# Kernel optimization log

Hardware: AMD Instinct MI355X
Metric: run time of the kernel (lower is better)

The kernel has to match this reference:

```python
import jax, jax.numpy as jnp
import numpy as np

EPS = 1e-5

def _bn(x, g, b):
    # BatchNorm3d in training mode over (batch, spatial) dims; x: [B, C, N]
    mean = jnp.mean(x, axis=(0, 2), keepdims=True)
    var = jnp.var(x, axis=(0, 2), keepdims=True)
    return g[None, :, None] * (x - mean) * jax.lax.rsqrt(var + EPS) + b[None, :, None]


def setup_inputs() -> dict:
    key = jax.random.key(0)
    ks = jax.random.split(key, 6)
    B, C, N, K, H = 2, 128, 32768, 9, 512
    x = jax.random.normal(ks[0], (B, C, N, 1), dtype=jnp.float32)
    edge_index = jax.random.randint(ks[1], (2, B, N, K), 0, N, dtype=jnp.int32)
    s = 0.05
    return {
        "x": x,
        "edge_index": edge_index,
        "w_mr": jax.random.normal(ks[2], (C, 2 * C), dtype=jnp.float32) * s,
        "b_mr": jnp.zeros((C,), jnp.float32),
        "g_mr": jnp.ones((C,), jnp.float32),
        "be_mr": jnp.zeros((C,), jnp.float32),
        "w1": jax.random.normal(ks[3], (H, C), dtype=jnp.float32) * s,
        "b1": jnp.zeros((H,), jnp.float32),
        "g1": jnp.ones((H,), jnp.float32),
        "be1": jnp.zeros((H,), jnp.float32),
        "w2": jax.random.normal(ks[4], (C, H), dtype=jnp.float32) * s,
        "b2": jnp.zeros((C,), jnp.float32),
        "g2": jnp.ones((C,), jnp.float32),
        "be2": jnp.zeros((C,), jnp.float32),
    }


def reference(x, edge_index, w_mr, b_mr, g_mr, be_mr, w1, b1, g1, be1, w2, b2, g2, be2):
    # x: [B, C, N, 1], edge_index: [2, B, N, K]
    B, C, N, _ = x.shape
    x2 = x[..., 0]  # [B, C, N]

    # batched_index_select: gather node features along N for each (B, N, K) index
    gather = jax.vmap(lambda xb, ib: xb[:, ib])  # ([C,N],[N,K]) -> [C,N,K]
    x_i = gather(x2, edge_index[1])  # [B, C, N, K] center features
    x_j = gather(x2, edge_index[0])  # [B, C, N, K] neighbor features
    rel = jnp.max(x_j - x_i, axis=-1)  # max-relative reduction -> [B, C, N]

    # torch.cat([x.unsqueeze(2), rel.unsqueeze(2)], 2).reshape(B, 2C, N): interleaved channels
    feat = jnp.stack([x2, rel], axis=2).reshape(B, 2 * C, N)

    # BasicConv([2C, C]): Conv3d 1x1 -> BN -> ReLU
    y = jnp.einsum('oc,bcn->bon', w_mr, feat) + b_mr[None, :, None]
    y = jax.nn.relu(_bn(y, g_mr, be_mr))

    # FFN: conv1x1 C->H, BN, ReLU, conv1x1 H->C, BN, residual
    h = jnp.einsum('hc,bcn->bhn', w1, y) + b1[None, :, None]
    h = jax.nn.relu(_bn(h, g1, be1))
    out = jnp.einsum('ch,bhn->bcn', w2, h) + b2[None, :, None]
    out = _bn(out, g2, be2) + y
    return out  # [B, C, N]
```

## Files before the change

### kernel.cpp

```cpp
#include <hip/hip_runtime.h>
#include <hip/hip_bf16.h>
#include <cstddef>
#include <cstdint>

#define BB 2
#define CC 128
#define NN 32768
#define KNBR 9
#define HH 512
#define PP (BB * NN)
#define TWO_C 256
#define EPSBN 1e-5f

typedef __attribute__((ext_vector_type(4))) float f32x4;
typedef __attribute__((ext_vector_type(8))) short s16x8;

__device__ __forceinline__ float bf2f(unsigned int u) {
    return __uint_as_float(u << 16);
}
__device__ __forceinline__ unsigned short f2bf(float f) {
    unsigned int u = __float_as_uint(f);
    u += 0x7fffu + ((u >> 16) & 1u);
    return (unsigned short)(u >> 16);
}

__device__ __forceinline__ s16x8 bnrelu(s16x8 v, f32x4 sa0, f32x4 sa1,
                                        f32x4 sb0, f32x4 sb1) {
    union { s16x8 s; __hip_bfloat162 h[4]; } u;
    u.s = v;
#pragma unroll
    for (int q = 0; q < 4; q++) {
        const float2 f = __bfloat1622float2(u.h[q]);
        const float slo = (q < 2) ? sa0[2 * q] : sa1[2 * q - 4];
        const float shi = (q < 2) ? sa0[2 * q + 1] : sa1[2 * q - 3];
        const float tlo = (q < 2) ? sb0[2 * q] : sb1[2 * q - 4];
        const float thi = (q < 2) ? sb0[2 * q + 1] : sb1[2 * q - 3];
        u.h[q] = __float22bfloat162_rn(make_float2(
            fmaxf(fmaf(slo, f.x, tlo), 0.f), fmaxf(fmaf(shi, f.y, thi), 0.f)));
    }
    return u.s;
}


__global__ __launch_bounds__(256) void transpose_wconv_kernel(
    const float* __restrict__ x, unsigned short* __restrict__ xT,
    const float* __restrict__ w_mr, const float* __restrict__ w1,
    const float* __restrict__ w2, unsigned short* __restrict__ o_mr,
    unsigned short* __restrict__ o1, unsigned short* __restrict__ o2) {
    if (blockIdx.x >= NN / 32) {
        if (blockIdx.y != 0) return;
        const int t = (blockIdx.x - NN / 32) * 256 + threadIdx.x;
        const float* src; unsigned short* dst; int K; int slot;
        if (t < 8192) { src = w1; dst = o1; K = 128; slot = t; }
        else if (t < 16384) { src = w2; dst = o2; K = 512; slot = t - 8192; }
        else if (t < 20480) { src = w_mr; dst = o_mr; K = 256; slot = t - 16384; }
        else return;
        const int lane = slot & 63;
        const int kt = (slot >> 6) % (K / 32);
        const int ot = (slot >> 6) / (K / 32);
        const int oc = ot * 16 + (lane & 15);
        const int k0 = kt * 32 + (lane >> 4) * 8;
        s16x8 v;
#pragma unroll
        for (int j = 0; j < 8; j++) v[j] = (short)f2bf(src[(size_t)oc * K + k0 + j]);
        *(s16x8*)(dst + (size_t)slot * 8) = v;
        return;
    }
    __shared__ float t[32][129];
    const int b = blockIdx.y;
    const int n0 = blockIdx.x * 32;
    const int tid = threadIdx.x;
    {
        const int tn = tid % 32;
        const int cq = tid / 32;
        for (int c = cq; c < CC; c += 8)
            t[tn][c] = x[((size_t)b * CC + c) * NN + n0 + tn];
    }
    __syncthreads();
    {
        const int ct = tid % 128;
        const int nq = tid / 128;
        for (int nl = nq; nl < 32; nl += 2)
            xT[((size_t)b * NN + n0 + nl) * CC + ct] = f2bf(t[nl][ct]);
    }
}

__global__ __launch_bounds__(256) void gather_kernel(
    const unsigned short* __restrict__ xT, const int* __restrict__ ei,
    unsigned short* __restrict__ feat) {
    __shared__ unsigned short lds[16 * 264];
    const int p0 = blockIdx.x * 16;
    const int b = p0 >> 15;
    const int n0 = p0 & (NN - 1);
    const int tid = threadIdx.x;
    const int wv = tid >> 6, lane = tid & 63;
    const unsigned short* xb = xT + (size_t)b * NN * CC;

#pragma unroll
    for (int q = 0; q < 4; q++) {
        const int pl = wv * 4 + q;
        const int n = n0 + pl;
        const int* e0 = ei + ((size_t)b * NN + n) * KNBR;
        const int* e1 = ei + ((size_t)(BB + b) * NN + n) * KNBR;
        const unsigned int xv = *(const unsigned int*)(xb + (size_t)n * CC + lane * 2);
        float m0 = -INFINITY, m1 = -INFINITY;
#pragma unroll
        for (int k = 0; k < KNBR; k++) {
            const int j0 = e0[k], j1 = e1[k];
            const unsigned int va = *(const unsigned int*)(xb + (size_t)j0 * CC + lane * 2);
            const unsigned int vb = *(const unsigned int*)(xb + (size_t)j1 * CC + lane * 2);
            m0 = fmaxf(m0, bf2f(va & 0xffffu) - bf2f(vb & 0xffffu));
            m1 = fmaxf(m1, bf2f(va >> 16) - bf2f(vb >> 16));
        }
        ushort4 o;
        o.x = (unsigned short)(xv & 0xffffu);
        o.y = f2bf(m0);
        o.z = (unsigned short)(xv >> 16);
        o.w = f2bf(m1);
        *(ushort4*)(lds + pl * 264 + lane * 4) = o;
    }
    __syncthreads();
#pragma unroll
    for (int pass = 0; pass < 2; pass++) {
        const int s = pass * 256 + tid;
        const int kt = s >> 6, ln = s & 63;
        const int pl = ln & 15, kq = ln >> 4;
        const s16x8 v = *(const s16x8*)(lds + pl * 264 + kt * 32 + kq * 8);
        *(s16x8*)(feat + ((size_t)((p0 >> 4) * 8 + kt) * 64 + ln) * 8) = v;
    }
}

template <int KTOT, int OCB, int OC, bool ACT>
__global__ __launch_bounds__(256, 2) void sgemm2_kernel(
    const unsigned short* __restrict__ A,
    const unsigned short* __restrict__ W,
    const float* __restrict__ bias,
    const float* __restrict__ act,
    unsigned short* __restrict__ Cout,
    float* __restrict__ part) {
    constexpr int KT = KTOT / 32;
    constexpr int NTB = OCB / 16;
    constexpr int NTW = NTB / 2;
    constexpr int OCT32 = OC / 32;

    __shared__ __align__(16) unsigned short ALDS[4 * KT * 512];
    __shared__ float bs[4 * OCB];

    const int tid = threadIdx.x;
    const int w = tid >> 6, lane = tid & 63;
    const int mw = w >> 1, nw = w & 1;
    const int lm = lane & 15, lg = lane >> 4;
    const int pt0 = blockIdx.x * 4;
    const int ob = blockIdx.y * OCB;

    {
        const unsigned short* Asrc = A + (size_t)pt0 * KT * 512;
        s16x8 ar[KT];
#pragma unroll
        for (int i = 0; i < KT; i++)
            ar[i] = *(const s16x8*)(Asrc + (size_t)(i * 256 + tid) * 8);
        if (ACT) {
#pragma unroll
            for (int i = 0; i < KT; i++) {
                const int s = i * 256 + tid;
                const int kts = (s >> 6) % KT;
                const int lgs = (s & 63) >> 4;
                const int ke = kts * 32 + lgs * 8;
                const f32x4 xa0 = *(const f32x4*)(act + ke);
                const f32x4 xa1 = *(const f32x4*)(act + ke + 4);
                const f32x4 xb0 = *(const f32x4*)(act + KTOT + ke);
                const f32x4 xb1 = *(const f32x4*)(act + KTOT + ke + 4);
                ar[i] = bnrelu(ar[i], xa0, xa1, xb0, xb1);
            }
        }
#pragma unroll
        for (int i = 0; i < KT; i++)
            *(s16x8*)(ALDS + (size_t)(i * 256 + tid) * 8) = ar[i];
    }
    __syncthreads();

    f32x4 acc[2][NTW] = {};

#pragma unroll
    for (int kt = 0; kt < KT; kt++) {
        s16x8 bF[NTW];
#pragma unroll
        for (int n = 0; n < NTW; n++)
            bF[n] = *(const s16x8*)(
                W + ((size_t)(((ob >> 4) + nw * NTW + n) * KT + kt) * 64 + lane) * 8);
        const s16x8 a0 = *(const s16x8*)(ALDS + (size_t)(((mw * 2 + 0) * KT + kt) * 64 + lane) * 8);
        const s16x8 a1 = *(const s16x8*)(ALDS + (size_t)(((mw * 2 + 1) * KT + kt) * 64 + lane) * 8);
#pragma unroll
        for (int n = 0; n < NTW; n++) {
            acc[0][n] = __builtin_amdgcn_mfma_f32_16x16x32_bf16(a0, bF[n], acc[0][n], 0, 0, 0);
            acc[1][n] = __builtin_amdgcn_mfma_f32_16x16x32_bf16(a1, bF[n], acc[1][n], 0, 0, 0);
        }
    }
    __syncthreads();

    unsigned short* myct = ALDS + (size_t)w * (NTW / 2) * 512;
    float sA[NTW], sB[NTW], bo[NTW];
#pragma unroll
    for (int n = 0; n < NTW; n++) {
        sA[n] = 0.f; sB[n] = 0.f;
        bo[n] = bias[ob + nw * (OCB / 2) + n * 16 + lm];
    }
#pragma unroll
    for (int mi = 0; mi < 2; mi++) {
        const int ptile = pt0 + mw * 2 + mi;
#pragma unroll
        for (int n = 0; n < NTW; n++) {
            const int lbase = ((n & 1) * 2 + (lm >> 3)) * 16 + lg * 4;
            const int elem = lm & 7;
#pragma unroll
            for (int j = 0; j < 4; j++) {
                const float h = acc[mi][n][j] + bo[n];
                sA[n] += h;
                sB[n] = fmaf(h, h, sB[n]);
                myct[(size_t)((n >> 1) * 64 + lbase + j) * 8 + elem] = f2bf(h);
            }
        }
#pragma unroll
        for (int og = 0; og < NTW / 2; og++) {
            const s16x8 v = *(const s16x8*)(myct + (size_t)(og * 64 + lane) * 8);
            const int oct = ((ob + nw * (OCB / 2)) >> 5) + og;
            *(s16x8*)(Cout + ((size_t)(ptile * OCT32 + oct) * 64 + lane) * 8) = v;
        }
    }
#pragma unroll
    for (int n = 0; n < NTW; n++) {
        float a = sA[n], q = sB[n];
        a += __shfl_xor(a, 16); a += __shfl_xor(a, 32);
        q += __shfl_xor(q, 16); q += __shfl_xor(q, 32);
        if (lg == 0) {
            const int chl = nw * (OCB / 2) + n * 16 + lm;
            bs[(mw * 2 + 0) * OCB + chl] = a;
            bs[(mw * 2 + 1) * OCB + chl] = q;
        }
    }
    __syncthreads();
    if (tid < OCB) {
        const float s = bs[0 * OCB + tid] + bs[2 * OCB + tid];
        const float q = bs[1 * OCB + tid] + bs[3 * OCB + tid];
        const size_t o = ((size_t)blockIdx.y * gridDim.x + blockIdx.x) * 2 * OCB;
        part[o + tid] = s;
        part[o + OCB + tid] = q;
    }
}

template <int OCB, int GX>
__global__ __launch_bounds__(256) void reduce_kernel(
    const float* __restrict__ part, const float* __restrict__ g,
    const float* __restrict__ be, float* __restrict__ act, int OC, float invP) {
    __shared__ float ls[4], lq[4];
    const int c = blockIdx.x;
    const int by = c / OCB, co = c % OCB;
    const int tid = threadIdx.x;
    float s = 0.f, q = 0.f;
#pragma unroll
    for (int i = 0; i < GX / 256; i++) {
        const int bx = i * 256 + tid;
        const size_t o = (size_t)(by * GX + bx) * 2 * OCB;
        s += part[o + co];
        q += part[o + OCB + co];
    }
#pragma unroll
    for (int off = 32; off >= 1; off >>= 1) {
        s += __shfl_xor(s, off);
        q += __shfl_xor(q, off);
    }
    if ((tid & 63) == 0) { ls[tid >> 6] = s; lq[tid >> 6] = q; }
    __syncthreads();
    if (tid == 0) {
        s = ls[0] + ls[1] + ls[2] + ls[3];
        q = lq[0] + lq[1] + lq[2] + lq[3];
        const float mean = s * invP;
        const float var = q * invP - mean * mean;
        const float a = g[c] * rsqrtf(var + EPSBN);
        act[c] = a;
        act[OC + c] = be[c] - mean * a;
    }
}

__global__ __launch_bounds__(256) void final_kernel(
    const unsigned short* __restrict__ yF, const unsigned short* __restrict__ oF,
    const float* __restrict__ act1, const float* __restrict__ act3,
    float* __restrict__ out) {
    __shared__ float t[32][132];
    const int p0 = blockIdx.x * 32;
    const int b = p0 >> 15;
    const int n0 = p0 & (NN - 1);
    const int tid = threadIdx.x;
#pragma unroll
    for (int s = tid; s < 512; s += 256) {
        const int pt = s >> 8;
        const int kt = (s >> 6) & 3;
        const int lane = s & 63;
        const int nl = pt * 16 + (lane & 15);
        const int c0 = kt * 32 + (lane >> 4) * 8;
        const size_t off = ((size_t)(((p0 >> 4) + pt) * 4 + kt) * 64 + lane) * 8;
        const s16x8 yv = *(const s16x8*)(yF + off);
        const s16x8 ov = *(const s16x8*)(oF + off);
        const f32x4 a1lo = *(const f32x4*)(act1 + c0);
        const f32x4 a1hi = *(const f32x4*)(act1 + c0 + 4);
        const f32x4 b1lo = *(const f32x4*)(act1 + CC + c0);
        const f32x4 b1hi = *(const f32x4*)(act1 + CC + c0 + 4);
        const f32x4 a3lo = *(const f32x4*)(act3 + c0);
        const f32x4 a3hi = *(const f32x4*)(act3 + c0 + 4);
        const f32x4 b3lo = *(const f32x4*)(act3 + CC + c0);
        const f32x4 b3hi = *(const f32x4*)(act3 + CC + c0 + 4);
#pragma unroll
        for (int j = 0; j < 8; j++) {
            const float yf = bf2f((unsigned short)yv[j]);
            const float of = bf2f((unsigned short)ov[j]);
            const float a1 = (j < 4) ? a1lo[j] : a1hi[j - 4];
            const float b1 = (j < 4) ? b1lo[j] : b1hi[j - 4];
            const float a3 = (j < 4) ? a3lo[j] : a3hi[j - 4];
            const float b3 = (j < 4) ? b3lo[j] : b3hi[j - 4];
            t[nl][c0 + j] = fmaf(a3, of, b3) + fmaxf(fmaf(a1, yf, b1), 0.f);
        }
    }
    __syncthreads();
    const int tn = tid & 31;
    const int cq = tid >> 5;
    for (int c = cq; c < CC; c += 8)
        out[((size_t)b * CC + c) * NN + n0 + tn] = t[tn][c];
}

extern "C" void kernel_launch(void* const* d_in, const int* in_sizes, int n_in,
                              void* d_out, int out_size, void* d_ws, size_t ws_size,
                              hipStream_t stream) {
    const float* x     = (const float*)d_in[0];
    const int*   ei    = (const int*)d_in[1];
    const float* w_mr  = (const float*)d_in[2];
    const float* b_mr  = (const float*)d_in[3];
    const float* g_mr  = (const float*)d_in[4];
    const float* be_mr = (const float*)d_in[5];
    const float* w1    = (const float*)d_in[6];
    const float* b1    = (const float*)d_in[7];
    const float* g1    = (const float*)d_in[8];
    const float* be1   = (const float*)d_in[9];
    const float* w2    = (const float*)d_in[10];
    const float* b2    = (const float*)d_in[11];
    const float* g2    = (const float*)d_in[12];
    const float* be2   = (const float*)d_in[13];
    float* out = (float*)d_out;

    char* ws = (char*)d_ws;
    unsigned short* xT    = (unsigned short*)(ws + 0);
    unsigned short* featF = (unsigned short*)(ws + 16777216);
    unsigned short* yF    = (unsigned short*)(ws + 50331648);
    unsigned short* hF    = (unsigned short*)(ws + 67108864);
    unsigned short* oF    = (unsigned short*)(ws + 134217728);
    unsigned short* wmrF  = (unsigned short*)(ws + 150994944);
    unsigned short* w1F   = (unsigned short*)(ws + 151060480);
    unsigned short* w2F   = (unsigned short*)(ws + 151191552);
    float* act1  = (float*)(ws + 151322624);
    float* act2  = (float*)(ws + 151323648);
    float* act3  = (float*)(ws + 151327744);
    float* part1 = (float*)(ws + 67108864);
    float* part2 = (float*)(ws + 134217728);
    float* part3 = (float*)(ws + 16777216);

    const float invP = 1.0f / (float)PP;

    transpose_wconv_kernel<<<dim3(NN / 32 + 80, BB), 256, 0, stream>>>(
        x, xT, w_mr, w1, w2, wmrF, w1F, w2F);
    gather_kernel<<<PP / 16, 256, 0, stream>>>(xT, ei, featF);

    sgemm2_kernel<TWO_C, CC, CC, false><<<dim3(PP / 64, 1), 256, 0, stream>>>(
        featF, wmrF, b_mr, act1, yF, part1);
    reduce_kernel<CC, PP / 64><<<CC, 256, 0, stream>>>(
        part1, g_mr, be_mr, act1, CC, invP);

    sgemm2_kernel<CC, 256, HH, true><<<dim3(PP / 64, 2), 256, 0, stream>>>(
        yF, w1F, b1, act1, hF, part2);
    reduce_kernel<256, PP / 64><<<HH, 256, 0, stream>>>(
        part2, g1, be1, act2, HH, invP);

    sgemm2_kernel<HH, CC, CC, true><<<dim3(PP / 64, 1), 256, 0, stream>>>(
        hF, w2F, b2, act2, oF, part3);
    reduce_kernel<CC, PP / 64><<<CC, 256, 0, stream>>>(
        part3, g2, be2, act3, CC, invP);

    final_kernel<<<PP / 32, 256, 0, stream>>>(yF, oF, act1, act3, out);
}
```

Baseline: 152.7 us.

## Fuse neighbor gather/max-relative into first GEMM kernel via LDS staging

Replaces the separate gather kernel and first sgemm with one kernel that computes the max-relative features for 64 points into shared memory, then runs the MFMA GEMM against the mr weights and emits BN partial sums. This removes the write and re-read of the 2C-wide feature buffer in global memory and one launch. In exchange each block serializes gather latency before its MFMA work, with fewer blocks (PP/64 instead of PP/16) to hide the irregular gather loads.

```diff
diff --git a/kernel.cpp b/kernel.cpp
--- a/kernel.cpp
+++ b/kernel.cpp
@@ -85,48 +85,131 @@
     }
 }
 
-__global__ __launch_bounds__(256) void gather_kernel(
+__global__ __launch_bounds__(256, 2) void ggemm1_kernel(
     const unsigned short* __restrict__ xT, const int* __restrict__ ei,
-    unsigned short* __restrict__ feat) {
-    __shared__ unsigned short lds[16 * 264];
-    const int p0 = blockIdx.x * 16;
+    const unsigned short* __restrict__ W,
+    const float* __restrict__ bias,
+    unsigned short* __restrict__ Cout,
+    float* __restrict__ part) {
+    constexpr int KT = TWO_C / 32;
+    constexpr int NTW = 4;
+    constexpr int OCT32 = CC / 32;
+
+    __shared__ __align__(16) unsigned short ALDS[4 * KT * 512];
+    __shared__ __align__(16) unsigned short scr[16 * 264];
+    __shared__ float bs[4 * CC];
+
+    const int tid = threadIdx.x;
+    const int w = tid >> 6, lane = tid & 63;
+    const int mw = w >> 1, nw = w & 1;
+    const int lm = lane & 15, lg = lane >> 4;
+    const int p0 = blockIdx.x * 64;
     const int b = p0 >> 15;
     const int n0 = p0 & (NN - 1);
-    const int tid = threadIdx.x;
-    const int wv = tid >> 6, lane = tid & 63;
+    const int pt0 = blockIdx.x * 4;
     const unsigned short* xb = xT + (size_t)b * NN * CC;
 
-#pragma unroll
-    for (int q = 0; q < 4; q++) {
-        const int pl = wv * 4 + q;
-        const int n = n0 + pl;
-        const int* e0 = ei + ((size_t)b * NN + n) * KNBR;
-        const int* e1 = ei + ((size_t)(BB + b) * NN + n) * KNBR;
-        const unsigned int xv = *(const unsigned int*)(xb + (size_t)n * CC + lane * 2);
-        float m0 = -INFINITY, m1 = -INFINITY;
-#pragma unroll
-        for (int k = 0; k < KNBR; k++) {
-            const int j0 = e0[k], j1 = e1[k];
-            const unsigned int va = *(const unsigned int*)(xb + (size_t)j0 * CC + lane * 2);
-            const unsigned int vb = *(const unsigned int*)(xb + (size_t)j1 * CC + lane * 2);
-            m0 = fmaxf(m0, bf2f(va & 0xffffu) - bf2f(vb & 0xffffu));
-            m1 = fmaxf(m1, bf2f(va >> 16) - bf2f(vb >> 16));
-        }
-        ushort4 o;
-        o.x = (unsigned short)(xv & 0xffffu);
-        o.y = f2bf(m0);
-        o.z = (unsigned short)(xv >> 16);
-        o.w = f2bf(m1);
-        *(ushort4*)(lds + pl * 264 + lane * 4) = o;
-    }
-    __syncthreads();
-#pragma unroll
-    for (int pass = 0; pass < 2; pass++) {
-        const int s = pass * 256 + tid;
-        const int kt = s >> 6, ln = s & 63;
-        const int pl = ln & 15, kq = ln >> 4;
-        const s16x8 v = *(const s16x8*)(lds + pl * 264 + kt * 32 + kq * 8);
-        *(s16x8*)(feat + ((size_t)((p0 >> 4) * 8 + kt) * 64 + ln) * 8) = v;
+    for (int it = 0; it < 4; it++) {
+#pragma unroll
+        for (int q = 0; q < 4; q++) {
+            const int spl = w * 4 + q;
+            const int n = n0 + it * 16 + spl;
+            const int* e0 = ei + ((size_t)b * NN + n) * KNBR;
+            const int* e1 = ei + ((size_t)(BB + b) * NN + n) * KNBR;
+            const unsigned int xv = *(const unsigned int*)(xb + (size_t)n * CC + lane * 2);
+            float m0 = -INFINITY, m1 = -INFINITY;
+#pragma unroll
+            for (int k = 0; k < KNBR; k++) {
+                const int j0 = e0[k], j1 = e1[k];
+                const unsigned int va = *(const unsigned int*)(xb + (size_t)j0 * CC + lane * 2);
+                const unsigned int vb = *(const unsigned int*)(xb + (size_t)j1 * CC + lane * 2);
+                m0 = fmaxf(m0, bf2f(va & 0xffffu) - bf2f(vb & 0xffffu));
+                m1 = fmaxf(m1, bf2f(va >> 16) - bf2f(vb >> 16));
+            }
+            ushort4 o;
+            o.x = (unsigned short)(xv & 0xffffu);
+            o.y = f2bf(m0);
+            o.z = (unsigned short)(xv >> 16);
+            o.w = f2bf(m1);
+            *(ushort4*)(scr + spl * 264 + lane * 4) = o;
+        }
+        __syncthreads();
+#pragma unroll
+        for (int pass = 0; pass < 2; pass++) {
+            const int s = pass * 256 + tid;
+            const int kt = s >> 6, ln = s & 63;
+            const int spl = ln & 15, kq = ln >> 4;
+            const s16x8 v = *(const s16x8*)(scr + spl * 264 + kt * 32 + kq * 8);
+            *(s16x8*)(ALDS + (size_t)((it * KT + kt) * 64 + ln) * 8) = v;
+        }
+        __syncthreads();
+    }
+
+    f32x4 acc[2][NTW] = {};
+#pragma unroll
+    for (int kt = 0; kt < KT; kt++) {
+        s16x8 bF[NTW];
+#pragma unroll
+        for (int n = 0; n < NTW; n++)
+            bF[n] = *(const s16x8*)(
+                W + ((size_t)((nw * NTW + n) * KT + kt) * 64 + lane) * 8);
+        const s16x8 a0 = *(const s16x8*)(ALDS + (size_t)(((mw * 2 + 0) * KT + kt) * 64 + lane) * 8);
+        const s16x8 a1 = *(const s16x8*)(ALDS + (size_t)(((mw * 2 + 1) * KT + kt) * 64 + lane) * 8);
+#pragma unroll
+        for (int n = 0; n < NTW; n++) {
+            acc[0][n] = __builtin_amdgcn_mfma_f32_16x16x32_bf16(a0, bF[n], acc[0][n], 0, 0, 0);
+            acc[1][n] = __builtin_amdgcn_mfma_f32_16x16x32_bf16(a1, bF[n], acc[1][n], 0, 0, 0);
+        }
+    }
+    __syncthreads();
+
+    unsigned short* myct = ALDS + (size_t)w * (NTW / 2) * 512;
+    float sA[NTW], sB[NTW], bo[NTW];
+#pragma unroll
+    for (int n = 0; n < NTW; n++) {
+        sA[n] = 0.f; sB[n] = 0.f;
+        bo[n] = bias[nw * 64 + n * 16 + lm];
+    }
+#pragma unroll
+    for (int mi = 0; mi < 2; mi++) {
+        const int ptile = pt0 + mw * 2 + mi;
+#pragma unroll
+        for (int n = 0; n < NTW; n++) {
+            const int lbase = ((n & 1) * 2 + (lm >> 3)) * 16 + lg * 4;
+            const int elem = lm & 7;
+#pragma unroll
+            for (int j = 0; j < 4; j++) {
+                const float h = acc[mi][n][j] + bo[n];
+                sA[n] += h;
+                sB[n] = fmaf(h, h, sB[n]);
+                myct[(size_t)((n >> 1) * 64 + lbase + j) * 8 + elem] = f2bf(h);
+            }
+        }
+#pragma unroll
+        for (int og = 0; og < NTW / 2; og++) {
+            const s16x8 v = *(const s16x8*)(myct + (size_t)(og * 64 + lane) * 8);
+            const int oct = (nw * 64 >> 5) + og;
+            *(s16x8*)(Cout + ((size_t)(ptile * OCT32 + oct) * 64 + lane) * 8) = v;
+        }
+    }
+#pragma unroll
+    for (int n = 0; n < NTW; n++) {
+        float a = sA[n], q = sB[n];
+        a += __shfl_xor(a, 16); a += __shfl_xor(a, 32);
+        q += __shfl_xor(q, 16); q += __shfl_xor(q, 32);
+        if (lg == 0) {
+            const int chl = nw * 64 + n * 16 + lm;
+            bs[(mw * 2 + 0) * CC + chl] = a;
+            bs[(mw * 2 + 1) * CC + chl] = q;
+        }
+    }
+    __syncthreads();
+    if (tid < CC) {
+        const float s = bs[0 * CC + tid] + bs[2 * CC + tid];
+        const float q = bs[1 * CC + tid] + bs[3 * CC + tid];
+        const size_t o = (size_t)blockIdx.x * 2 * CC;
+        part[o + tid] = s;
+        part[o + CC + tid] = q;
     }
 }
 
@@ -348,7 +431,6 @@
 
     char* ws = (char*)d_ws;
     unsigned short* xT    = (unsigned short*)(ws + 0);
-    unsigned short* featF = (unsigned short*)(ws + 16777216);
     unsigned short* yF    = (unsigned short*)(ws + 50331648);
     unsigned short* hF    = (unsigned short*)(ws + 67108864);
     unsigned short* oF    = (unsigned short*)(ws + 134217728);
@@ -366,10 +448,8 @@
 
     transpose_wconv_kernel<<<dim3(NN / 32 + 80, BB), 256, 0, stream>>>(
         x, xT, w_mr, w1, w2, wmrF, w1F, w2F);
-    gather_kernel<<<PP / 16, 256, 0, stream>>>(xT, ei, featF);
-
-    sgemm2_kernel<TWO_C, CC, CC, false><<<dim3(PP / 64, 1), 256, 0, stream>>>(
-        featF, wmrF, b_mr, act1, yF, part1);
+
+    ggemm1_kernel<<<PP / 64, 256, 0, stream>>>(xT, ei, wmrF, b_mr, yF, part1);
     reduce_kernel<CC, PP / 64><<<CC, 256, 0, stream>>>(
         part1, g_mr, be_mr, act1, CC, invP);
 
```

After: 225.2 us. 1.47x slower.
